# Kernel optimization log

Hardware: AMD Instinct MI355X
Metric: run time of the kernel (lower is better)

The kernel has to match this reference:

```python
import jax, jax.numpy as jnp
import numpy as np


def conv3d(x, w, b):
    # x: [B,C,D,H,W], w: [O,I,3,3,3], padding=1, stride=1
    y = jax.lax.conv_general_dilated(
        x, w, window_strides=(1, 1, 1), padding=[(1, 1)] * 3,
        dimension_numbers=("NCDHW", "OIDHW", "NCDHW"))
    return y + b[None, :, None, None, None]


def trilinear_sample(x, cd, ch, cw):
    # x: [B,C,D,H,W]; cd/ch/cw: [B,K,D,H,W] float sampling coords.
    # Zero padding outside the volume (invalid corners masked to 0).
    B, C, D, H, W = x.shape
    d0 = jnp.floor(cd); h0 = jnp.floor(ch); w0 = jnp.floor(cw)
    fd, fh, fw = cd - d0, ch - h0, cw - w0
    d0 = d0.astype(jnp.int32); h0 = h0.astype(jnp.int32); w0 = w0.astype(jnp.int32)
    gather = jax.vmap(lambda xb, z, y, xx: xb[:, z, y, xx])  # -> [B,C,K,D,H,W]
    out = jnp.zeros((B, C) + cd.shape[1:], x.dtype)
    for dz in (0, 1):
        wz = fd if dz else 1.0 - fd
        zi = d0 + dz
        for dy in (0, 1):
            wy = fh if dy else 1.0 - fh
            yi = h0 + dy
            for dx in (0, 1):
                wx = fw if dx else 1.0 - fw
                xi = w0 + dx
                valid = ((zi >= 0) & (zi < D) & (yi >= 0) & (yi < H)
                         & (xi >= 0) & (xi < W)).astype(x.dtype)
                v = gather(x, jnp.clip(zi, 0, D - 1), jnp.clip(yi, 0, H - 1),
                           jnp.clip(xi, 0, W - 1))
                out = out + (wz * wy * wx * valid)[:, None] * v
    return out


def deform_conv3d(x, offsets, mask, w, b):
    # Modulated deformable 3D conv (DCNv2-style), kernel 3x3x3, pad 1, stride 1.
    # offsets: [B,81,D,H,W] = 27 taps x (dd,dh,dw); mask: [B,27,D,H,W].
    B, C, D, H, W = x.shape
    K = 27
    off = offsets.reshape(B, K, 3, D, H, W)
    kd, kh, kw = jnp.meshgrid(jnp.arange(3), jnp.arange(3), jnp.arange(3), indexing="ij")
    tap_d = (kd.reshape(-1) - 1).astype(x.dtype)[None, :, None, None, None]
    tap_h = (kh.reshape(-1) - 1).astype(x.dtype)[None, :, None, None, None]
    tap_w = (kw.reshape(-1) - 1).astype(x.dtype)[None, :, None, None, None]
    gd = jnp.arange(D, dtype=x.dtype)[None, None, :, None, None]
    gh = jnp.arange(H, dtype=x.dtype)[None, None, None, :, None]
    gw = jnp.arange(W, dtype=x.dtype)[None, None, None, None, :]
    cd = gd + tap_d + off[:, :, 0]
    ch = gh + tap_h + off[:, :, 1]
    cw = gw + tap_w + off[:, :, 2]
    sampled = trilinear_sample(x, cd, ch, cw) * mask[:, None]  # [B,C,K,D,H,W]
    out = jnp.einsum("bckdhw,ock->bodhw", sampled, w.reshape(w.shape[0], C, K))
    return out + b[None, :, None, None, None]


def mdconv3d(x, ow, ob, w, b):
    # MDConv3d: internal offset/mask predictor + modulated deformable conv.
    d = conv3d(x, ow, ob)
    offsets, mask = d[:, :81], jax.nn.sigmoid(d[:, 81:])
    return deform_conv3d(x, offsets, mask, w, b)


def forward(x, ow1, ob1, w1, b1, ow2, ob2, w2, b2, ow3, ob3, w3, b3,
            defo_w, defo_b, c3d_w, c3d_b):
    h = jax.nn.relu(mdconv3d(x, ow1, ob1, w1, b1))
    h = jax.nn.relu(mdconv3d(h, ow2, ob2, w2, b2))
    h = jax.nn.relu(mdconv3d(h, ow3, ob3, w3, b3))
    d = conv3d(h, defo_w, defo_b)
    offsets, alpha = d[:, :81], jax.nn.sigmoid(d[:, 81:])
    return deform_conv3d(x, offsets, alpha, c3d_w, c3d_b)


def setup_inputs() -> dict:
    key = jax.random.key(0)
    ks = jax.random.split(key, 16)
    B, C, D, H, W = 1, 256, 8, 32, 32
    M = 256  # mdim
    OFF_SCALE = 0.02  # small init so predicted offsets stay moderate

    def p(k, shape):
        return jax.random.normal(k, shape, jnp.float32) * OFF_SCALE

    inp = {"x": jax.random.normal(ks[0], (B, C, D, H, W), jnp.float32)}
    c_ins = [C, M, M]
    for i, cin in enumerate(c_ins, 1):
        inp[f"ow{i}"] = p(ks[2 * i - 1], (108, cin, 3, 3, 3))
        inp[f"ob{i}"] = jnp.zeros((108,), jnp.float32)
        inp[f"w{i}"] = p(ks[2 * i], (M, cin, 3, 3, 3))
        inp[f"b{i}"] = jnp.zeros((M,), jnp.float32)
    inp["defo_w"] = p(ks[13], (108, M, 3, 3, 3))
    inp["defo_b"] = jnp.zeros((108,), jnp.float32)
    inp["c3d_w"] = p(ks[14], (256, C, 3, 3, 3))
    inp["c3d_b"] = jnp.zeros((256,), jnp.float32)
    return inp


def reference(x, ow1, ob1, w1, b1, ow2, ob2, w2, b2, ow3, ob3, w3, b3,
              defo_w, defo_b, c3d_w, c3d_b):
    return forward(x, ow1, ob1, w1, b1, ow2, ob2, w2, b2, ow3, ob3, w3, b3,
                   defo_w, defo_b, c3d_w, c3d_b)
```

## Files before the change

kernel.cpp:

```cpp
#include <hip/hip_runtime.h>
#include <cstdint>

#define NPOS 8192
#define KTOT 6912
#define XP_ROWS 11560
#define XP_SY 34
#define XP_SZ 1156
#define KS 4
#define KSL 1728
#define NCHUNK 27

typedef float  facc_t __attribute__((ext_vector_type(4)));
typedef short  bf8_t  __attribute__((ext_vector_type(8)));
typedef unsigned short ub8_t __attribute__((ext_vector_type(8)));

__device__ __forceinline__ unsigned short f2bf(float f) {
    unsigned u = __float_as_uint(f);
    u = (u + 0x7FFFu + ((u >> 16) & 1u)) >> 16;
    return (unsigned short)u;
}
__device__ __forceinline__ float bf2f(unsigned short u) {
    return __uint_as_float(((unsigned)u) << 16);
}

__global__ __launch_bounds__(256) void zero_k(unsigned short* __restrict__ dst) {
    ub8_t zz = {0,0,0,0,0,0,0,0};
    *(ub8_t*)&dst[((size_t)blockIdx.x * 256 + threadIdx.x) * 8] = zz;
}

__global__ __launch_bounds__(256) void pad_x_t(const float* __restrict__ x,
                                               unsigned short* __restrict__ XpA) {
    __shared__ unsigned short T[256 * 33];
    int b = blockIdx.x;
    int z = b >> 5, y = b & 31;
    int t = threadIdx.x;
    int c8 = t >> 5, xv = t & 31;
#pragma unroll 4
    for (int i = 0; i < 32; ++i) {
        int c = i * 8 + c8;
        T[c * 33 + xv] = f2bf(x[c * NPOS + (z << 10) + (y << 5) + xv]);
    }
    __syncthreads();
    int rowb = ((z + 1) * XP_SZ + (y + 1) * XP_SY + 1) * 256;
#pragma unroll 4
    for (int j = 0; j < 32; ++j) {
        XpA[rowb + j * 256 + t] = T[t * 33 + j];
    }
}

__global__ __launch_bounds__(256) void wtrans_all(
    const float* __restrict__ o1, const float* __restrict__ o2,
    const float* __restrict__ o3, const float* __restrict__ o4,
    const float* __restrict__ m1, const float* __restrict__ m2,
    const float* __restrict__ m3, const float* __restrict__ m4,
    unsigned short* __restrict__ wtoff, unsigned short* __restrict__ wtmain) {
    __shared__ float T[6912];
    int b = blockIdx.x, t = threadIdx.x;
    const float* src; unsigned short* dst; int o, O;
    if (b < 512) {
        int L = b >> 7; o = b & 127; O = 108;
        src = (L == 0) ? o1 : (L == 1) ? o2 : (L == 2) ? o3 : o4;
        dst = wtoff + ((size_t)(L * 128 + o)) * KTOT;
    } else {
        int b2 = b - 512;
        int L = b2 >> 8; o = b2 & 255; O = 256;
        src = (L == 0) ? m1 : (L == 1) ? m2 : (L == 2) ? m3 : m4;
        dst = wtmain + ((size_t)(L * 256 + o)) * KTOT;
    }
    if (o < O) {
#pragma unroll 3
        for (int i = 0; i < 27; ++i) T[i * 256 + t] = src[(size_t)o * KTOT + i * 256 + t];
        __syncthreads();
#pragma unroll 3
        for (int i = 0; i < 27; ++i) {
            int kc = i * 256 + t;
            int c = kc & 255, k = kc >> 8;
            dst[kc] = f2bf(T[c * 27 + k]);
        }
    } else {
#pragma unroll 3
        for (int i = 0; i < 27; ++i) dst[i * 256 + t] = 0;
    }
}

template<bool DEFORM>
__global__ __launch_bounds__(256, 2)
void fgemm(const unsigned short* __restrict__ Xp,
           const unsigned short* __restrict__ wt,
           const float* __restrict__ dbuf,
           float* __restrict__ parts) {
    constexpr int O   = DEFORM ? 256 : 128;
    constexpr int PWN = DEFORM ? 4 : 2;
    __shared__ unsigned short Bs[64 * 64] __attribute__((aligned(16)));

    const int t = threadIdx.x;
    const int wave = t >> 6, lane = t & 63;
    const int q = lane >> 4, r = lane & 15;

    const int bid = blockIdx.x + (blockIdx.y << 7);
    const int xcd = bid & 7;
    const int idx = bid >> 3;
    const int pt  = (xcd << 4) | (idx & 15);
    const int ks  = idx >> 4;
    const int pbase = pt * 64;
    const int kstart = ks * KSL;

    const int obw = DEFORM ? (wave * 64) : ((wave >> 1) * 64);
    const int pfb = DEFORM ? 0 : ((wave & 1) * 32);

    const int pl = t >> 2;
    const int csub = (t & 3) * 16;
    const int p = pbase + pl;
    const int z = p >> 10, y = (p >> 5) & 31, xx = p & 31;
    const int g0 = (t & 3) * 2;
    const int wr0 = pl * 64 + ((g0 ^ (pl & 7)) << 3);
    const int wr1 = pl * 64 + (((g0 + 1) ^ (pl & 7)) << 3);

    facc_t acc[4][PWN];
#pragma unroll
    for (int i = 0; i < 4; ++i)
#pragma unroll
        for (int ip = 0; ip < PWN; ++ip) acc[i][ip] = (facc_t){0.f, 0.f, 0.f, 0.f};

    float cw[8];
    int row0 = 0;
    int ktap = -1;
    ub8_t stv[16];
    ub8_t scv0, scv1;
    float dn0 = 0.f, dn1 = 0.f, dn2 = 0.f, dn3 = 0.f;

    auto comp_tap = [&](int k_s, float od, float oh, float ow_, float m) {
        const int kd = k_s / 9, kh = (k_s / 3) % 3, kw = k_s % 3;
        float cd = (float)(z + kd - 1) + od;
        float ch = (float)(y + kh - 1) + oh;
        float cx = (float)(xx + kw - 1) + ow_;
        float fdf = floorf(cd), fhf = floorf(ch), fwf = floorf(cx);
        float fd = cd - fdf, fh = ch - fhf, fw = cx - fwf;
        float wz0 = 1.f - fd, wz1 = fd;
        float wy0 = 1.f - fh, wy1 = fh;
        float wx0 = 1.f - fw, wx1 = fw;
        int id, ih, iw;
        if (fdf < -1.f || fdf >= 8.f)  { wz0 = 0.f; wz1 = 0.f; id = 0; } else id = (int)fdf;
        if (fhf < -1.f || fhf >= 32.f) { wy0 = 0.f; wy1 = 0.f; ih = 0; } else ih = (int)fhf;
        if (fwf < -1.f || fwf >= 32.f) { wx0 = 0.f; wx1 = 0.f; iw = 0; } else iw = (int)fwf;
        wz0 *= m; wz1 *= m;
        float w00 = wz0 * wy0, w01 = wz0 * wy1, w10 = wz1 * wy0, w11 = wz1 * wy1;
        cw[0] = w00 * wx0; cw[1] = w00 * wx1;
        cw[2] = w01 * wx0; cw[3] = w01 * wx1;
        cw[4] = w10 * wx0; cw[5] = w10 * wx1;
        cw[6] = w11 * wx0; cw[7] = w11 * wx1;
        row0 = (id + 1) * XP_SZ + (ih + 1) * XP_SY + (iw + 1);
    };
    auto pref_tap = [&](int kn) {
        dn0 = dbuf[(3 * kn + 0) * NPOS + p];
        dn1 = dbuf[(3 * kn + 1) * NPOS + p];
        dn2 = dbuf[(3 * kn + 2) * NPOS + p];
        dn3 = dbuf[(81 + kn) * NPOS + p];
    };
    auto issue_gathers = [&](int c0_s) {
        const unsigned short* cb = Xp + (size_t)row0 * 256 + c0_s + csub;
#pragma unroll
        for (int j = 0; j < 8; ++j) {
            const int roff = ((j >> 2) & 1) * XP_SZ + ((j >> 1) & 1) * XP_SY + (j & 1);
            stv[2 * j]     = *(const ub8_t*)(cb + roff * 256);
            stv[2 * j + 1] = *(const ub8_t*)(cb + roff * 256 + 8);
        }
    };
    auto conv_issue = [&](int kc_s) {
        const int k_s = kc_s >> 8, c0_s = kc_s & 255;
        const int kd = k_s / 9, kh = (k_s / 3) % 3, kw = k_s % 3;
        const int row = (z + kd) * XP_SZ + (y + kh) * XP_SY + (xx + kw);
        scv0 = *(const ub8_t*)&Xp[(size_t)row * 256 + c0_s + csub];
        scv1 = *(const ub8_t*)&Xp[(size_t)row * 256 + c0_s + csub + 8];
    };

    if (DEFORM) {
        ktap = kstart >> 8;
        comp_tap(ktap, dbuf[(3 * ktap + 0) * NPOS + p], dbuf[(3 * ktap + 1) * NPOS + p],
                 dbuf[(3 * ktap + 2) * NPOS + p], dbuf[(81 + ktap) * NPOS + p]);
        pref_tap(ktap + 1 > 26 ? 26 : ktap + 1);
        issue_gathers(kstart & 255);
    } else {
        conv_issue(kstart);
    }

    for (int chunk = 0; chunk < NCHUNK; ++chunk) {
        const int kc0 = kstart + chunk * 64;
        const int c0 = kc0 & 255; (void)c0;

        bf8_t afr[2][4];
#pragma unroll
        for (int sl = 0; sl < 2; ++sl)
#pragma unroll
            for (int i = 0; i < 4; ++i)
                afr[sl][i] = *(const bf8_t*)&wt[(size_t)(obw + i * 16 + r) * KTOT + kc0 + sl * 32 + q * 8];

        if (DEFORM) {
            float av[16];
#pragma unroll
            for (int e = 0; e < 16; ++e) av[e] = 0.f;
#pragma unroll
            for (int j = 0; j < 8; ++j) {
#pragma unroll
                for (int e = 0; e < 8; ++e) {
                    av[e]     += cw[j] * bf2f(stv[2 * j][e]);
                    av[8 + e] += cw[j] * bf2f(stv[2 * j + 1][e]);
                }
            }
            ub8_t v0, v1;
#pragma unroll
            for (int e = 0; e < 8; ++e) { v0[e] = f2bf(av[e]); v1[e] = f2bf(av[8 + e]); }
            if (chunk + 1 < NCHUNK) {
                const int kc1 = kc0 + 64;
                const int k1 = kc1 >> 8;
                if (k1 != ktap) {
                    ktap = k1;
                    comp_tap(k1, dn0, dn1, dn2, dn3);
                    pref_tap(k1 + 1 > 26 ? 26 : k1 + 1);
                }
                issue_gathers(kc1 & 255);
            }
            *(ub8_t*)&Bs[wr0] = v0;
            *(ub8_t*)&Bs[wr1] = v1;
        } else {
            *(ub8_t*)&Bs[wr0] = scv0;
            *(ub8_t*)&Bs[wr1] = scv1;
            if (chunk + 1 < NCHUNK) conv_issue(kc0 + 64);
        }

        asm volatile("s_waitcnt lgkmcnt(0)" ::: "memory");
        __builtin_amdgcn_s_barrier();
        __builtin_amdgcn_sched_barrier(0);

#pragma unroll
        for (int sl = 0; sl < 2; ++sl) {
            bf8_t bfr[PWN];
#pragma unroll
            for (int ip = 0; ip < PWN; ++ip) {
                int brow = pfb + ip * 16 + r;
                bfr[ip] = *(const bf8_t*)&Bs[brow * 64 + (((sl * 4 + q) ^ (brow & 7)) << 3)];
            }
#pragma unroll
            for (int i = 0; i < 4; ++i)
#pragma unroll
                for (int ip = 0; ip < PWN; ++ip)
                    acc[i][ip] = __builtin_amdgcn_mfma_f32_16x16x32_bf16(afr[sl][i], bfr[ip], acc[i][ip], 0, 0, 0);
        }

        __builtin_amdgcn_s_barrier();
        __builtin_amdgcn_sched_barrier(0);
    }

    float* pp = parts + (size_t)ks * O * NPOS;
#pragma unroll
    for (int i = 0; i < 4; ++i)
#pragma unroll
        for (int ip = 0; ip < PWN; ++ip)
#pragma unroll
            for (int reg = 0; reg < 4; ++reg) {
                int o = obw + i * 16 + q * 4 + reg;
                int px = pbase + pfb + ip * 16 + r;
                pp[(size_t)o * NPOS + px] = acc[i][ip][reg];
            }
}

__global__ __launch_bounds__(256) void ccombine(const float* __restrict__ parts,
                                                const float* __restrict__ ob,
                                                float* __restrict__ dbuf) {
    int b = blockIdx.x;
    int o = b >> 3;
    int p4 = ((b & 7) * 256 + threadIdx.x) * 4;
    float s0 = 0, s1 = 0, s2 = 0, s3 = 0;
#pragma unroll
    for (int s = 0; s < KS; ++s) {
        const float4 v = *(const float4*)&parts[((size_t)(s * 128 + o)) * NPOS + p4];
        s0 += v.x; s1 += v.y; s2 += v.z; s3 += v.w;
    }
    float bv = ob[o];
    s0 += bv; s1 += bv; s2 += bv; s3 += bv;
    if (o >= 81) {
        s0 = 1.f / (1.f + __expf(-s0));
        s1 = 1.f / (1.f + __expf(-s1));
        s2 = 1.f / (1.f + __expf(-s2));
        s3 = 1.f / (1.f + __expf(-s3));
    }
    *(float4*)&dbuf[(size_t)o * NPOS + p4] = make_float4(s0, s1, s2, s3);
}

__global__ __launch_bounds__(256) void dcombine_h(const float* __restrict__ parts,
                                                  const float* __restrict__ bias,
                                                  unsigned short* __restrict__ XpB) {
    __shared__ unsigned short T[64 * 66];
    int p0 = blockIdx.x * 64, o0 = blockIdx.y * 64;
    int t = threadIdx.x;
    int pl = t & 63, og = t >> 6;
#pragma unroll 4
    for (int j = 0; j < 16; ++j) {
        int ol = og * 16 + j;
        float s = 0.f;
#pragma unroll
        for (int sp = 0; sp < KS; ++sp)
            s += parts[((size_t)(sp * 256 + o0 + ol)) * NPOS + p0 + pl];
        s += bias[o0 + ol];
        T[ol * 66 + pl] = f2bf(fmaxf(s, 0.f));
    }
    __syncthreads();
    int c = t & 63, pr = t >> 6;
#pragma unroll 4
    for (int j = 0; j < 16; ++j) {
        int pl2 = j * 4 + pr;
        int pg = p0 + pl2;
        int zz = pg >> 10, yy = (pg >> 5) & 31, xv = pg & 31;
        int row = (zz + 1) * XP_SZ + (yy + 1) * XP_SY + xv + 1;
        XpB[(size_t)row * 256 + o0 + c] = T[c * 66 + pl2];
    }
}

__global__ __launch_bounds__(256) void dcombine_out(const float* __restrict__ parts,
                                                    const float* __restrict__ bias,
                                                    float* __restrict__ out) {
    int b = blockIdx.x;
    int o = b >> 3;
    int p4 = ((b & 7) * 256 + threadIdx.x) * 4;
    float s0 = 0, s1 = 0, s2 = 0, s3 = 0;
#pragma unroll
    for (int s = 0; s < KS; ++s) {
        const float4 v = *(const float4*)&parts[((size_t)(s * 256 + o)) * NPOS + p4];
        s0 += v.x; s1 += v.y; s2 += v.z; s3 += v.w;
    }
    float bv = bias[o];
    *(float4*)&out[(size_t)o * NPOS + p4] = make_float4(s0 + bv, s1 + bv, s2 + bv, s3 + bv);
}

extern "C" void kernel_launch(void* const* d_in, const int* in_sizes, int n_in,
                              void* d_out, int out_size, void* d_ws, size_t ws_size,
                              hipStream_t stream) {
    const float* x      = (const float*)d_in[0];
    const float* ow1    = (const float*)d_in[1];
    const float* ob1    = (const float*)d_in[2];
    const float* w1     = (const float*)d_in[3];
    const float* b1     = (const float*)d_in[4];
    const float* ow2    = (const float*)d_in[5];
    const float* ob2    = (const float*)d_in[6];
    const float* w2     = (const float*)d_in[7];
    const float* b2     = (const float*)d_in[8];
    const float* ow3    = (const float*)d_in[9];
    const float* ob3    = (const float*)d_in[10];
    const float* w3     = (const float*)d_in[11];
    const float* b3     = (const float*)d_in[12];
    const float* defo_w = (const float*)d_in[13];
    const float* defo_b = (const float*)d_in[14];
    const float* c3d_w  = (const float*)d_in[15];
    const float* c3d_b  = (const float*)d_in[16];
    float* out = (float*)d_out;

    unsigned short* XpA    = (unsigned short*)d_ws;
    unsigned short* XpB    = XpA + (size_t)XP_ROWS * 256;
    unsigned short* wtoff  = XpB + (size_t)XP_ROWS * 256;
    unsigned short* wtmain = wtoff + (size_t)4 * 128 * KTOT;
    float* dbufp = (float*)(wtmain + (size_t)4 * 256 * KTOT);
    float* parts = dbufp + (size_t)108 * NPOS;

    const dim3 blk(256);
    const dim3 gG(128, KS);

    zero_k<<<2890, blk, 0, stream>>>(XpA);
    pad_x_t<<<256, blk, 0, stream>>>(x, XpA);
    wtrans_all<<<1536, blk, 0, stream>>>(ow1, ow2, ow3, defo_w, w1, w2, w3, c3d_w, wtoff, wtmain);

    const float* cbias[4] = {ob1, ob2, ob3, defo_b};
    const float* dbias[4] = {b1, b2, b3, c3d_b};

    for (int L = 0; L < 4; ++L) {
        const unsigned short* featConv = (L == 0) ? XpA : XpB;
        const unsigned short* featDef  = (L == 3) ? XpA : featConv;
        fgemm<false><<<gG, blk, 0, stream>>>(featConv, wtoff + (size_t)L * 128 * KTOT, nullptr, parts);
        ccombine<<<864, blk, 0, stream>>>(parts, cbias[L], dbufp);
        fgemm<true><<<gG, blk, 0, stream>>>(featDef, wtmain + (size_t)L * 256 * KTOT, dbufp, parts);
        if (L < 3) dcombine_h<<<dim3(128, 4), blk, 0, stream>>>(parts, dbias[L], XpB);
        else       dcombine_out<<<2048, blk, 0, stream>>>(parts, dbias[L], out);
    }
}
```

Before: 738.2 us.

## Double-buffer deformable gathers two chunks ahead in the fused conv kernel

The deformable path now keeps two register sets of gathered corner values and blend weights (A/B), so the gathers for chunk c+2 are issued while chunk c is blended and its MFMAs run. This lengthens the prefetch distance to hide global-gather latency. In exchange it roughly doubles the gather staging registers (about 32 extra VGPRs plus weights), which can lower occupancy or cause spills. The plain-conv path is only reorganised into helper lambdas.

```diff
diff --git a/kernel.cpp b/kernel.cpp
--- a/kernel.cpp
+++ b/kernel.cpp
@@ -125,7 +125,8 @@
     float cw[8];
     int row0 = 0;
     int ktap = -1;
-    ub8_t stv[16];
+    ub8_t stvA[16], stvB[16];
+    float cwA[8], cwB[8];
     ub8_t scv0, scv1;
     float dn0 = 0.f, dn1 = 0.f, dn2 = 0.f, dn3 = 0.f;
 
@@ -157,14 +158,40 @@
         dn2 = dbuf[(3 * kn + 2) * NPOS + p];
         dn3 = dbuf[(81 + kn) * NPOS + p];
     };
-    auto issue_gathers = [&](int c0_s) {
-        const unsigned short* cb = Xp + (size_t)row0 * 256 + c0_s + csub;
+    auto issue_to = [&](ub8_t (&sv)[16], float (&cwd)[8], int kc_s) {
+        const int k1 = kc_s >> 8;
+        if (k1 != ktap) {
+            ktap = k1;
+            comp_tap(k1, dn0, dn1, dn2, dn3);
+            pref_tap(k1 + 1 > 26 ? 26 : k1 + 1);
+        }
+#pragma unroll
+        for (int j = 0; j < 8; ++j) cwd[j] = cw[j];
+        const unsigned short* cb = Xp + (size_t)row0 * 256 + (kc_s & 255) + csub;
 #pragma unroll
         for (int j = 0; j < 8; ++j) {
             const int roff = ((j >> 2) & 1) * XP_SZ + ((j >> 1) & 1) * XP_SY + (j & 1);
-            stv[2 * j]     = *(const ub8_t*)(cb + roff * 256);
-            stv[2 * j + 1] = *(const ub8_t*)(cb + roff * 256 + 8);
-        }
+            sv[2 * j]     = *(const ub8_t*)(cb + roff * 256);
+            sv[2 * j + 1] = *(const ub8_t*)(cb + roff * 256 + 8);
+        }
+    };
+    auto blend_write = [&](ub8_t (&sv)[16], float (&cwd)[8]) {
+        float av[16];
+#pragma unroll
+        for (int e = 0; e < 16; ++e) av[e] = 0.f;
+#pragma unroll
+        for (int j = 0; j < 8; ++j) {
+#pragma unroll
+            for (int e = 0; e < 8; ++e) {
+                av[e]     += cwd[j] * bf2f(sv[2 * j][e]);
+                av[8 + e] += cwd[j] * bf2f(sv[2 * j + 1][e]);
+            }
+        }
+        ub8_t v0, v1;
+#pragma unroll
+        for (int e = 0; e < 8; ++e) { v0[e] = f2bf(av[e]); v1[e] = f2bf(av[8 + e]); }
+        *(ub8_t*)&Bs[wr0] = v0;
+        *(ub8_t*)&Bs[wr1] = v1;
     };
     auto conv_issue = [&](int kc_s) {
         const int k_s = kc_s >> 8, c0_s = kc_s & 255;
@@ -173,65 +200,14 @@
         scv0 = *(const ub8_t*)&Xp[(size_t)row * 256 + c0_s + csub];
         scv1 = *(const ub8_t*)&Xp[(size_t)row * 256 + c0_s + csub + 8];
     };
-
-    if (DEFORM) {
-        ktap = kstart >> 8;
-        comp_tap(ktap, dbuf[(3 * ktap + 0) * NPOS + p], dbuf[(3 * ktap + 1) * NPOS + p],
-                 dbuf[(3 * ktap + 2) * NPOS + p], dbuf[(81 + ktap) * NPOS + p]);
-        pref_tap(ktap + 1 > 26 ? 26 : ktap + 1);
-        issue_gathers(kstart & 255);
-    } else {
-        conv_issue(kstart);
-    }
-
-    for (int chunk = 0; chunk < NCHUNK; ++chunk) {
-        const int kc0 = kstart + chunk * 64;
-        const int c0 = kc0 & 255; (void)c0;
-
-        bf8_t afr[2][4];
+    auto load_afr = [&](bf8_t (&af)[2][4], int kc0) {
 #pragma unroll
         for (int sl = 0; sl < 2; ++sl)
 #pragma unroll
             for (int i = 0; i < 4; ++i)
-                afr[sl][i] = *(const bf8_t*)&wt[(size_t)(obw + i * 16 + r) * KTOT + kc0 + sl * 32 + q * 8];
-
-        if (DEFORM) {
-            float av[16];
-#pragma unroll
-            for (int e = 0; e < 16; ++e) av[e] = 0.f;
-#pragma unroll
-            for (int j = 0; j < 8; ++j) {
-#pragma unroll
-                for (int e = 0; e < 8; ++e) {
-                    av[e]     += cw[j] * bf2f(stv[2 * j][e]);
-                    av[8 + e] += cw[j] * bf2f(stv[2 * j + 1][e]);
-                }
-            }
-            ub8_t v0, v1;
-#pragma unroll
-            for (int e = 0; e < 8; ++e) { v0[e] = f2bf(av[e]); v1[e] = f2bf(av[8 + e]); }
-            if (chunk + 1 < NCHUNK) {
-                const int kc1 = kc0 + 64;
-                const int k1 = kc1 >> 8;
-                if (k1 != ktap) {
-                    ktap = k1;
-                    comp_tap(k1, dn0, dn1, dn2, dn3);
-                    pref_tap(k1 + 1 > 26 ? 26 : k1 + 1);
-                }
-                issue_gathers(kc1 & 255);
-            }
-            *(ub8_t*)&Bs[wr0] = v0;
-            *(ub8_t*)&Bs[wr1] = v1;
-        } else {
-            *(ub8_t*)&Bs[wr0] = scv0;
-            *(ub8_t*)&Bs[wr1] = scv1;
-            if (chunk + 1 < NCHUNK) conv_issue(kc0 + 64);
-        }
-
-        asm volatile("s_waitcnt lgkmcnt(0)" ::: "memory");
-        __builtin_amdgcn_s_barrier();
-        __builtin_amdgcn_sched_barrier(0);
-
+                af[sl][i] = *(const bf8_t*)&wt[(size_t)(obw + i * 16 + r) * KTOT + kc0 + sl * 32 + q * 8];
+    };
+    auto do_mfma = [&](bf8_t (&af)[2][4]) {
 #pragma unroll
         for (int sl = 0; sl < 2; ++sl) {
             bf8_t bfr[PWN];
@@ -244,11 +220,74 @@
             for (int i = 0; i < 4; ++i)
 #pragma unroll
                 for (int ip = 0; ip < PWN; ++ip)
-                    acc[i][ip] = __builtin_amdgcn_mfma_f32_16x16x32_bf16(afr[sl][i], bfr[ip], acc[i][ip], 0, 0, 0);
-        }
-
+                    acc[i][ip] = __builtin_amdgcn_mfma_f32_16x16x32_bf16(af[sl][i], bfr[ip], acc[i][ip], 0, 0, 0);
+        }
+    };
+    auto sync_pre = [&]() {
+        asm volatile("s_waitcnt lgkmcnt(0)" ::: "memory");
         __builtin_amdgcn_s_barrier();
         __builtin_amdgcn_sched_barrier(0);
+    };
+    auto sync_post = [&]() {
+        __builtin_amdgcn_s_barrier();
+        __builtin_amdgcn_sched_barrier(0);
+    };
+
+    if constexpr (DEFORM) {
+        const int tap0 = kstart >> 8;
+        ktap = tap0;
+        comp_tap(tap0, dbuf[(3 * tap0 + 0) * NPOS + p], dbuf[(3 * tap0 + 1) * NPOS + p],
+                 dbuf[(3 * tap0 + 2) * NPOS + p], dbuf[(81 + tap0) * NPOS + p]);
+        pref_tap(tap0 + 1 > 26 ? 26 : tap0 + 1);
+        {
+#pragma unroll
+            for (int j = 0; j < 8; ++j) cwA[j] = cw[j];
+            const unsigned short* cb = Xp + (size_t)row0 * 256 + (kstart & 255) + csub;
+#pragma unroll
+            for (int j = 0; j < 8; ++j) {
+                const int roff = ((j >> 2) & 1) * XP_SZ + ((j >> 1) & 1) * XP_SY + (j & 1);
+                stvA[2 * j]     = *(const ub8_t*)(cb + roff * 256);
+                stvA[2 * j + 1] = *(const ub8_t*)(cb + roff * 256 + 8);
+            }
+        }
+        issue_to(stvB, cwB, kstart + 64);
+
+        for (int c = 0; c < NCHUNK - 1; c += 2) {
+            bf8_t afr[2][4];
+            load_afr(afr, kstart + c * 64);
+            blend_write(stvA, cwA);
+            issue_to(stvA, cwA, kstart + (c + 2) * 64);
+            sync_pre();
+            do_mfma(afr);
+            sync_post();
+            load_afr(afr, kstart + (c + 1) * 64);
+            blend_write(stvB, cwB);
+            if (c + 3 < NCHUNK) issue_to(stvB, cwB, kstart + (c + 3) * 64);
+            sync_pre();
+            do_mfma(afr);
+            sync_post();
+        }
+        {
+            bf8_t afr[2][4];
+            load_afr(afr, kstart + (NCHUNK - 1) * 64);
+            blend_write(stvA, cwA);
+            sync_pre();
+            do_mfma(afr);
+            sync_post();
+        }
+    } else {
+        conv_issue(kstart);
+        for (int chunk = 0; chunk < NCHUNK; ++chunk) {
+            const int kc0 = kstart + chunk * 64;
+            bf8_t afr[2][4];
+            load_afr(afr, kc0);
+            *(ub8_t*)&Bs[wr0] = scv0;
+            *(ub8_t*)&Bs[wr1] = scv1;
+            if (chunk + 1 < NCHUNK) conv_issue(kc0 + 64);
+            sync_pre();
+            do_mfma(afr);
+            sync_post();
+        }
     }
 
     float* pp = parts + (size_t)ks * O * NPOS;
```

Measured after the change: 1.706 ms. 131% more time.

## Use 512-thread blocks for deformable GEMM, halving per-thread gather and output work

Applied to the files above, without the earlier changes.

The deformable fgemm now launches 512 threads (8 waves). Each wave owns 32 output channels instead of 64, and each thread gathers 8 channels per corner instead of 16 for one position. This halves per-thread registers (stv, av, acc) so more waves can be resident and the trilinear gather latency is better hidden. The cost is that each thread recomputes the tap coordinates and interpolation weights, so that work is duplicated, and A-fragment loads per block double.

```diff
diff --git a/kernel.cpp b/kernel.cpp
--- a/kernel.cpp
+++ b/kernel.cpp
@@ -84,12 +84,13 @@
 }
 
 template<bool DEFORM>
-__global__ __launch_bounds__(256, 2)
+__global__ __launch_bounds__(DEFORM ? 512 : 256, DEFORM ? 4 : 2)
 void fgemm(const unsigned short* __restrict__ Xp,
            const unsigned short* __restrict__ wt,
            const float* __restrict__ dbuf,
            float* __restrict__ parts) {
     constexpr int O   = DEFORM ? 256 : 128;
+    constexpr int IO  = DEFORM ? 2 : 4;
     constexpr int PWN = DEFORM ? 4 : 2;
     __shared__ unsigned short Bs[64 * 64] __attribute__((aligned(16)));
 
@@ -105,27 +106,28 @@
     const int pbase = pt * 64;
     const int kstart = ks * KSL;
 
-    const int obw = DEFORM ? (wave * 64) : ((wave >> 1) * 64);
+    const int obw = DEFORM ? (wave * 32) : ((wave >> 1) * 64);
     const int pfb = DEFORM ? 0 : ((wave & 1) * 32);
 
-    const int pl = t >> 2;
-    const int csub = (t & 3) * 16;
+    const int pl   = DEFORM ? (t >> 3) : (t >> 2);
+    const int csub = DEFORM ? ((t & 7) * 8) : ((t & 3) * 16);
     const int p = pbase + pl;
     const int z = p >> 10, y = (p >> 5) & 31, xx = p & 31;
+    const int wrD = pl * 64 + (((t & 7) ^ (pl & 7)) << 3);
     const int g0 = (t & 3) * 2;
     const int wr0 = pl * 64 + ((g0 ^ (pl & 7)) << 3);
     const int wr1 = pl * 64 + (((g0 + 1) ^ (pl & 7)) << 3);
 
-    facc_t acc[4][PWN];
-#pragma unroll
-    for (int i = 0; i < 4; ++i)
+    facc_t acc[IO][PWN];
+#pragma unroll
+    for (int i = 0; i < IO; ++i)
 #pragma unroll
         for (int ip = 0; ip < PWN; ++ip) acc[i][ip] = (facc_t){0.f, 0.f, 0.f, 0.f};
 
     float cw[8];
     int row0 = 0;
     int ktap = -1;
-    ub8_t stv[16];
+    ub8_t stv[8];
     ub8_t scv0, scv1;
     float dn0 = 0.f, dn1 = 0.f, dn2 = 0.f, dn3 = 0.f;
 
@@ -162,8 +164,7 @@
 #pragma unroll
         for (int j = 0; j < 8; ++j) {
             const int roff = ((j >> 2) & 1) * XP_SZ + ((j >> 1) & 1) * XP_SY + (j & 1);
-            stv[2 * j]     = *(const ub8_t*)(cb + roff * 256);
-            stv[2 * j + 1] = *(const ub8_t*)(cb + roff * 256 + 8);
+            stv[j] = *(const ub8_t*)(cb + roff * 256);
         }
     };
     auto conv_issue = [&](int kc_s) {
@@ -186,30 +187,27 @@
 
     for (int chunk = 0; chunk < NCHUNK; ++chunk) {
         const int kc0 = kstart + chunk * 64;
-        const int c0 = kc0 & 255; (void)c0;
-
-        bf8_t afr[2][4];
+
+        bf8_t afr[2][IO];
 #pragma unroll
         for (int sl = 0; sl < 2; ++sl)
 #pragma unroll
-            for (int i = 0; i < 4; ++i)
+            for (int i = 0; i < IO; ++i)
                 afr[sl][i] = *(const bf8_t*)&wt[(size_t)(obw + i * 16 + r) * KTOT + kc0 + sl * 32 + q * 8];
 
         if (DEFORM) {
-            float av[16];
-#pragma unroll
-            for (int e = 0; e < 16; ++e) av[e] = 0.f;
+            float av[8];
+#pragma unroll
+            for (int e = 0; e < 8; ++e) av[e] = 0.f;
 #pragma unroll
             for (int j = 0; j < 8; ++j) {
 #pragma unroll
-                for (int e = 0; e < 8; ++e) {
-                    av[e]     += cw[j] * bf2f(stv[2 * j][e]);
-                    av[8 + e] += cw[j] * bf2f(stv[2 * j + 1][e]);
-                }
+                for (int e = 0; e < 8; ++e)
+                    av[e] += cw[j] * bf2f(stv[j][e]);
             }
-            ub8_t v0, v1;
-#pragma unroll
-            for (int e = 0; e < 8; ++e) { v0[e] = f2bf(av[e]); v1[e] = f2bf(av[8 + e]); }
+            ub8_t v0;
+#pragma unroll
+            for (int e = 0; e < 8; ++e) v0[e] = f2bf(av[e]);
             if (chunk + 1 < NCHUNK) {
                 const int kc1 = kc0 + 64;
                 const int k1 = kc1 >> 8;
@@ -220,8 +218,7 @@
                 }
                 issue_gathers(kc1 & 255);
             }
-            *(ub8_t*)&Bs[wr0] = v0;
-            *(ub8_t*)&Bs[wr1] = v1;
+            *(ub8_t*)&Bs[wrD] = v0;
         } else {
             *(ub8_t*)&Bs[wr0] = scv0;
             *(ub8_t*)&Bs[wr1] = scv1;
@@ -241,7 +238,7 @@
                 bfr[ip] = *(const bf8_t*)&Bs[brow * 64 + (((sl * 4 + q) ^ (brow & 7)) << 3)];
             }
 #pragma unroll
-            for (int i = 0; i < 4; ++i)
+            for (int i = 0; i < IO; ++i)
 #pragma unroll
                 for (int ip = 0; ip < PWN; ++ip)
                     acc[i][ip] = __builtin_amdgcn_mfma_f32_16x16x32_bf16(afr[sl][i], bfr[ip], acc[i][ip], 0, 0, 0);
@@ -253,7 +250,7 @@
 
     float* pp = parts + (size_t)ks * O * NPOS;
 #pragma unroll
-    for (int i = 0; i < 4; ++i)
+    for (int i = 0; i < IO; ++i)
 #pragma unroll
         for (int ip = 0; ip < PWN; ++ip)
 #pragma unroll
@@ -362,6 +359,7 @@
     float* parts = dbufp + (size_t)108 * NPOS;
 
     const dim3 blk(256);
+    const dim3 blkD(512);
     const dim3 gG(128, KS);
 
     zero_k<<<2890, blk, 0, stream>>>(XpA);
@@ -376,7 +374,7 @@
         const unsigned short* featDef  = (L == 3) ? XpA : featConv;
         fgemm<false><<<gG, blk, 0, stream>>>(featConv, wtoff + (size_t)L * 128 * KTOT, nullptr, parts);
         ccombine<<<864, blk, 0, stream>>>(parts, cbias[L], dbufp);
-        fgemm<true><<<gG, blk, 0, stream>>>(featDef, wtmain + (size_t)L * 256 * KTOT, dbufp, parts);
+        fgemm<true><<<gG, blkD, 0, stream>>>(featDef, wtmain + (size_t)L * 256 * KTOT, dbufp, parts);
         if (L < 3) dcombine_h<<<dim3(128, 4), blk, 0, stream>>>(parts, dbias[L], XpB);
         else       dcombine_out<<<2048, blk, 0, stream>>>(parts, dbias[L], out);
     }
```

After: 732.0 us. About the same (-0.8%).
